# Kernel optimization log

Measured on AMD Instinct MI355X. Metric: run time of the kernel, lower is better.

## Reference

```python
import jax, jax.numpy as jnp
import numpy as np

N = 8192
D = 512


def setup_inputs() -> dict:
    key = jax.random.key(0)
    ks = jax.random.split(key, 7)
    X = jax.random.normal(ks[0], (N, D), dtype=jnp.float32)
    adj = jax.random.randint(ks[1], (N, N), 0, 2, dtype=jnp.int32)
    # guarantee at least one neighbor per row (self-loop) so softmax is defined
    adj = adj.at[jnp.arange(N), jnp.arange(N)].set(1)
    s = 1.0 / np.sqrt(D)
    Wq = jax.random.normal(ks[2], (D, D), dtype=jnp.float32) * s
    Wk = jax.random.normal(ks[3], (D, D), dtype=jnp.float32) * s
    Wv = jax.random.normal(ks[4], (D, D), dtype=jnp.float32) * s
    Wo = jax.random.normal(ks[5], (D, D), dtype=jnp.float32) * s
    bo = jnp.zeros((D,), dtype=jnp.float32)
    return {"X": X, "adj": adj, "Wq": Wq, "Wk": Wk, "Wv": Wv, "Wo": Wo, "bo": bo}


def reference(X, adj, Wq, Wk, Wv, Wo, bo):
    # torch Linear(no bias): y = x @ W.T
    Q = X @ Wq.T                                  # [N, D]
    K = X @ Wk.T                                  # [N, D]
    V = X @ Wv.T                                  # [N, D]
    scale = 1.0 / jnp.sqrt(jnp.asarray(D, X.dtype))
    scores = jnp.einsum('nd,md->nm', Q, K) * scale  # [N, N]
    scores = jnp.where(adj == 0, -jnp.inf, scores)
    attn = jax.nn.softmax(scores, axis=-1)          # [N, N]
    out = attn @ V                                  # [N, D]
    out = out @ Wo.T + bo                           # [N, D]
    return out
```

## Files before the change

### kernel.cpp

```cpp
#include <hip/hip_runtime.h>

namespace {

constexpr int NR = 8192;
constexpr int DD = 512;
constexpr int NSPLIT = 4;
constexpr int KVLEN = NR / NSPLIT;
constexpr int KT = 32;
constexpr int NT = KVLEN / KT;
constexpr int QB = 64;
constexpr float SCALE = 0.04419417382415922f;
constexpr float THR = 5.0f;

typedef __bf16 bf16x8 __attribute__((ext_vector_type(8)));
typedef __bf16 bf16x4 __attribute__((ext_vector_type(4)));
typedef float  f32x16 __attribute__((ext_vector_type(16)));

__device__ __forceinline__ f32x16 mfma(bf16x8 a, bf16x8 b, f32x16 c) {
    return __builtin_amdgcn_mfma_f32_32x32x16_bf16(a, b, c, 0, 0, 0);
}

__global__ void __launch_bounds__(256)
cast_kernel(const float* __restrict__ in, __bf16* __restrict__ out, int n8) {
    int i = blockIdx.x * 256 + threadIdx.x;
    if (i >= n8) return;
    const float4* p = (const float4*)(in + (size_t)i * 8);
    float4 v0 = p[0], v1 = p[1];
    bf16x8 o;
    o[0] = (__bf16)v0.x; o[1] = (__bf16)v0.y; o[2] = (__bf16)v0.z; o[3] = (__bf16)v0.w;
    o[4] = (__bf16)v1.x; o[5] = (__bf16)v1.y; o[6] = (__bf16)v1.z; o[7] = (__bf16)v1.w;
    *(bf16x8*)(out + (size_t)i * 8) = o;
}

template<bool FINAL>
__global__ void __launch_bounds__(256, 2)
gemm_kernel(const __bf16* __restrict__ A, const __bf16* __restrict__ B0,
            const __bf16* __restrict__ B1, const __bf16* __restrict__ B2,
            __bf16* __restrict__ C0, __bf16* __restrict__ C1, __bf16* __restrict__ C2,
            const float* __restrict__ bias, float* __restrict__ Cf)
{
    const __bf16* B = B0;
    __bf16* Cb = C0;
    if (!FINAL) {
        if (blockIdx.y == 1)      { B = B1; Cb = C1; }
        else if (blockIdx.y == 2) { B = B2; Cb = C2; }
    }
    __shared__ __bf16 As[128][72];
    __shared__ __bf16 Bs[128][72];
    const int t = threadIdx.x;
    const int w = t >> 6, lane = t & 63, lo = lane & 31, hi = lane >> 5;
    const int wm = w >> 1, wn = w & 1;
    const int bm = (blockIdx.x >> 2) * 128;
    const int bn = (blockIdx.x & 3) * 128;

    f32x16 acc[2][2];
    #pragma unroll
    for (int a = 0; a < 2; ++a)
        #pragma unroll
        for (int b = 0; b < 2; ++b)
            #pragma unroll
            for (int r = 0; r < 16; ++r) acc[a][b][r] = 0.f;

    for (int k0 = 0; k0 < DD; k0 += 64) {
        __syncthreads();
        #pragma unroll
        for (int pp = 0; pp < 2; ++pp) {
            int r = pp * 64 + (t >> 2), c = (t & 3) * 16;
            *(bf16x8*)&As[r][c]     = *(const bf16x8*)(A + (size_t)(bm + r) * DD + k0 + c);
            *(bf16x8*)&As[r][c + 8] = *(const bf16x8*)(A + (size_t)(bm + r) * DD + k0 + c + 8);
            *(bf16x8*)&Bs[r][c]     = *(const bf16x8*)(B + (size_t)(bn + r) * DD + k0 + c);
            *(bf16x8*)&Bs[r][c + 8] = *(const bf16x8*)(B + (size_t)(bn + r) * DD + k0 + c + 8);
        }
        __syncthreads();
        #pragma unroll
        for (int ks = 0; ks < 4; ++ks) {
            bf16x8 a0 = *(const bf16x8*)&As[wm * 64 + lo][ks * 16 + hi * 8];
            bf16x8 a1 = *(const bf16x8*)&As[wm * 64 + 32 + lo][ks * 16 + hi * 8];
            bf16x8 b0 = *(const bf16x8*)&Bs[wn * 64 + lo][ks * 16 + hi * 8];
            bf16x8 b1 = *(const bf16x8*)&Bs[wn * 64 + 32 + lo][ks * 16 + hi * 8];
            acc[0][0] = mfma(a0, b0, acc[0][0]);
            acc[0][1] = mfma(a0, b1, acc[0][1]);
            acc[1][0] = mfma(a1, b0, acc[1][0]);
            acc[1][1] = mfma(a1, b1, acc[1][1]);
        }
    }
    #pragma unroll
    for (int mi = 0; mi < 2; ++mi)
        #pragma unroll
        for (int ni = 0; ni < 2; ++ni) {
            int col = bn + wn * 64 + ni * 32 + lo;
            float bv = 0.f;
            if (FINAL) bv = bias[col];
            #pragma unroll
            for (int r = 0; r < 16; ++r) {
                int row = bm + wm * 64 + mi * 32 + (r & 3) + 8 * (r >> 2) + 4 * hi;
                if (FINAL) Cf[(size_t)row * DD + col] = acc[mi][ni][r] + bv;
                else       Cb[(size_t)row * DD + col] = (__bf16)acc[mi][ni][r];
            }
        }
}

__global__ void __launch_bounds__(256)
transpose_kernel(const __bf16* __restrict__ V, __bf16* __restrict__ Vt) {
    __shared__ __bf16 tile[64][72];
    const int t = threadIdx.x;
    const int rb = blockIdx.x * 64;
    const int cb = blockIdx.y * 64;
    #pragma unroll
    for (int pp = 0; pp < 2; ++pp) {
        int r = pp * 32 + (t >> 3), c = (t & 7) * 8;
        *(bf16x8*)&tile[r][c] = *(const bf16x8*)(V + (size_t)(rb + r) * DD + cb + c);
    }
    __syncthreads();
    #pragma unroll
    for (int pp = 0; pp < 2; ++pp) {
        int dd = pp * 32 + (t >> 3), co = (t & 7) * 8;
        bf16x8 o;
        #pragma unroll
        for (int j = 0; j < 8; ++j) o[j] = tile[co + j][dd];
        *(bf16x8*)(Vt + (size_t)(cb + dd) * NR + rb + co) = o;
    }
}

__global__ void __launch_bounds__(256, 2)
flash_kernel(const __bf16* __restrict__ Qg, const __bf16* __restrict__ Kg,
             const __bf16* __restrict__ Vt, const int* __restrict__ adj,
             __bf16* __restrict__ Opart, float* __restrict__ lse)
{
    __shared__ __bf16 Sp[4][QB][40];
    __shared__ __bf16 Pl[QB][40];
    __shared__ float  fl[QB];
    __shared__ float  ll[QB];
    __shared__ int    flg[4];

    const int t = threadIdx.x;
    const int w = t >> 6, lane = t & 63, lo = lane & 31, hi = lane >> 5;
    const int qblk = blockIdx.x * QB;
    const int split = blockIdx.y;
    const int kv0 = split * KVLEN;

    bf16x8 qa[2][8];
    #pragma unroll
    for (int mi = 0; mi < 2; ++mi)
        #pragma unroll
        for (int ks = 0; ks < 8; ++ks)
            qa[mi][ks] = *(const bf16x8*)(Qg + (size_t)(qblk + mi * 32 + lo) * DD + w * 128 + ks * 16 + hi * 8);

    f32x16 O[2][2][2];
    #pragma unroll
    for (int h = 0; h < 2; ++h)
        #pragma unroll
        for (int a = 0; a < 2; ++a)
            #pragma unroll
            for (int b = 0; b < 2; ++b)
                #pragma unroll
                for (int r = 0; r < 16; ++r) O[h][a][b][r] = 0.f;

    const __bf16* Kl = Kg + (size_t)(kv0 + lo) * DD + w * 128 + hi * 8;
    const __bf16* Vbase = Vt + (size_t)(w * 128 + lo) * NR + kv0 + hi * 8;

    const int qo = w * 16 + (lane >> 2);
    const int c8 = (lane & 3) * 8;
    const int* adjp = adj + (size_t)(qblk + qo) * NR + kv0 + c8;
    int4 aA = *(const int4*)adjp;
    int4 aB = *(const int4*)(adjp + 4);

    float m_run = -1e30f, l_run = 0.f;

    for (int tl = 0; tl < NT; ++tl) {
        f32x16 St0, St1;
        #pragma unroll
        for (int r = 0; r < 16; ++r) { St0[r] = 0.f; St1[r] = 0.f; }
        #pragma unroll
        for (int ks = 0; ks < 8; ++ks) {
            bf16x8 kb = *(const bf16x8*)(Kl + ks * 16);
            St0 = mfma(kb, qa[0][ks], St0);
            St1 = mfma(kb, qa[1][ks], St1);
        }
        Kl += KT * DD;
        #pragma unroll
        for (int g = 0; g < 4; ++g) {
            bf16x4 v0, v1;
            #pragma unroll
            for (int j = 0; j < 4; ++j) { v0[j] = (__bf16)St0[4 * g + j]; v1[j] = (__bf16)St1[4 * g + j]; }
            *(bf16x4*)&Sp[w][lo][8 * g + 4 * hi]      = v0;
            *(bf16x4*)&Sp[w][32 + lo][8 * g + 4 * hi] = v1;
        }
        __syncthreads();
        {
            bf16x8 p0 = *(const bf16x8*)&Sp[0][qo][c8];
            bf16x8 p1 = *(const bf16x8*)&Sp[1][qo][c8];
            bf16x8 p2 = *(const bf16x8*)&Sp[2][qo][c8];
            bf16x8 p3 = *(const bf16x8*)&Sp[3][qo][c8];
            int am[8] = {aA.x, aA.y, aA.z, aA.w, aB.x, aB.y, aB.z, aB.w};
            float s[8];
            #pragma unroll
            for (int i = 0; i < 8; ++i) {
                float v = ((float)p0[i] + (float)p1[i] + (float)p2[i] + (float)p3[i]) * SCALE;
                s[i] = (am[i] != 0) ? v : -1e30f;
            }
            float mx = s[0];
            #pragma unroll
            for (int i = 1; i < 8; ++i) mx = fmaxf(mx, s[i]);
            mx = fmaxf(mx, __shfl_xor(mx, 1));
            mx = fmaxf(mx, __shfl_xor(mx, 2));
            bool need = mx > m_run + THR;
            float m_new = need ? mx : m_run;
            float f = need ? __expf(m_run - m_new) : 1.f;
            float lsum = 0.f;
            bf16x8 pb;
            #pragma unroll
            for (int i = 0; i < 8; ++i) {
                float pv = __expf(s[i] - m_new);
                lsum += pv;
                pb[i] = (__bf16)pv;
            }
            lsum += __shfl_xor(lsum, 1);
            lsum += __shfl_xor(lsum, 2);
            l_run = l_run * f + lsum;
            m_run = m_new;
            *(bf16x8*)&Pl[qo][c8] = pb;
            if ((lane & 3) == 0) fl[qo] = f;
            unsigned long long bal = __ballot(need);
            if (lane == 0) flg[w] = (bal != 0ull) ? 1 : 0;
            int nxt = (tl + 1 < NT) ? (tl + 1) * KT : 0;
            aA = *(const int4*)(adjp + nxt);
            aB = *(const int4*)(adjp + nxt + 4);
        }
        __syncthreads();
        if (flg[0] | flg[1] | flg[2] | flg[3]) {
            #pragma unroll
            for (int mi = 0; mi < 2; ++mi)
                #pragma unroll
                for (int g = 0; g < 4; ++g) {
                    float4 fv = *(const float4*)&fl[mi * 32 + 8 * g + 4 * hi];
                    #pragma unroll
                    for (int j = 0; j < 4; ++j) {
                        float fac = (&fv.x)[j];
                        #pragma unroll
                        for (int h = 0; h < 2; ++h)
                            #pragma unroll
                            for (int ni = 0; ni < 2; ++ni)
                                O[h][mi][ni][g * 4 + j] *= fac;
                    }
                }
        }
        bf16x8 pa[2][2];
        #pragma unroll
        for (int mi = 0; mi < 2; ++mi)
            #pragma unroll
            for (int ks = 0; ks < 2; ++ks)
                pa[mi][ks] = *(const bf16x8*)&Pl[mi * 32 + lo][ks * 16 + hi * 8];
        const int vofs = tl * KT;
        #pragma unroll
        for (int h = 0; h < 2; ++h)
            #pragma unroll
            for (int ni = 0; ni < 2; ++ni) {
                const __bf16* vp = Vbase + (size_t)(h * 64 + ni * 32) * NR + vofs;
                bf16x8 vb0 = *(const bf16x8*)(vp);
                bf16x8 vb1 = *(const bf16x8*)(vp + 16);
                O[h][0][ni] = mfma(pa[0][0], vb0, O[h][0][ni]);
                O[h][1][ni] = mfma(pa[1][0], vb0, O[h][1][ni]);
                O[h][0][ni] = mfma(pa[0][1], vb1, O[h][0][ni]);
                O[h][1][ni] = mfma(pa[1][1], vb1, O[h][1][ni]);
            }
    }
    if ((lane & 3) == 0) {
        ll[qo] = l_run;
        lse[(size_t)split * NR + qblk + qo] = m_run + __logf(l_run);
    }
    __syncthreads();
    #pragma unroll
    for (int mi = 0; mi < 2; ++mi)
        #pragma unroll
        for (int g = 0; g < 4; ++g) {
            float4 lv = *(const float4*)&ll[mi * 32 + 8 * g + 4 * hi];
            #pragma unroll
            for (int j = 0; j < 4; ++j) {
                float inv = 1.f / (&lv.x)[j];
                int row = qblk + mi * 32 + 8 * g + 4 * hi + j;
                #pragma unroll
                for (int h = 0; h < 2; ++h)
                    #pragma unroll
                    for (int ni = 0; ni < 2; ++ni) {
                        int col = w * 128 + h * 64 + ni * 32 + lo;
                        Opart[(size_t)split * NR * DD + (size_t)row * DD + col] =
                            (__bf16)(O[h][mi][ni][g * 4 + j] * inv);
                    }
            }
        }
}

__global__ void __launch_bounds__(256)
merge_kernel(const __bf16* __restrict__ Opart, const float* __restrict__ lse,
             __bf16* __restrict__ attn)
{
    int idx = blockIdx.x * 256 + threadIdx.x;
    int q = idx >> 6;
    int c = (idx & 63) * 8;
    float l0 = lse[q], l1 = lse[NR + q], l2 = lse[2 * NR + q], l3 = lse[3 * NR + q];
    float M = fmaxf(fmaxf(l0, l1), fmaxf(l2, l3));
    float w0 = __expf(l0 - M), w1 = __expf(l1 - M), w2 = __expf(l2 - M), w3 = __expf(l3 - M);
    float Winv = 1.f / (w0 + w1 + w2 + w3);
    const size_t base = (size_t)q * DD + c;
    const size_t stride = (size_t)NR * DD;
    bf16x8 o0 = *(const bf16x8*)(Opart + base);
    bf16x8 o1 = *(const bf16x8*)(Opart + stride + base);
    bf16x8 o2 = *(const bf16x8*)(Opart + 2 * stride + base);
    bf16x8 o3 = *(const bf16x8*)(Opart + 3 * stride + base);
    bf16x8 o;
    #pragma unroll
    for (int i = 0; i < 8; ++i)
        o[i] = (__bf16)((w0 * (float)o0[i] + w1 * (float)o1[i] +
                         w2 * (float)o2[i] + w3 * (float)o3[i]) * Winv);
    *(bf16x8*)(attn + base) = o;
}

}

extern "C" void kernel_launch(void* const* d_in, const int* in_sizes, int n_in,
                              void* d_out, int out_size, void* d_ws, size_t ws_size,
                              hipStream_t stream)
{
    (void)in_sizes; (void)n_in; (void)out_size; (void)ws_size;
    const float* X  = (const float*)d_in[0];
    const int*   adj = (const int*)d_in[1];
    const float* Wq = (const float*)d_in[2];
    const float* Wk = (const float*)d_in[3];
    const float* Wv = (const float*)d_in[4];
    const float* Wo = (const float*)d_in[5];
    const float* bo = (const float*)d_in[6];
    float* out = (float*)d_out;

    char* ws = (char*)d_ws;
    __bf16* Xb   = (__bf16*)(ws + 0);
    __bf16* Att  = (__bf16*)(ws + 0);
    __bf16* Wqb  = (__bf16*)(ws + 8388608);
    __bf16* Wkb  = (__bf16*)(ws + 8912896);
    __bf16* Wvb  = (__bf16*)(ws + 9437184);
    __bf16* Wob  = (__bf16*)(ws + 9961472);
    __bf16* Qb   = (__bf16*)(ws + 10485760);
    __bf16* Kb   = (__bf16*)(ws + 18874368);
    __bf16* Vb   = (__bf16*)(ws + 27262976);
    __bf16* Vtb  = (__bf16*)(ws + 35651584);
    __bf16* Op   = (__bf16*)(ws + 44040192);
    float*  lseb = (float*)(ws + 77594624);

    cast_kernel<<<2048, 256, 0, stream>>>(X,  Xb,  NR * DD / 8);
    cast_kernel<<<128,  256, 0, stream>>>(Wq, Wqb, DD * DD / 8);
    cast_kernel<<<128,  256, 0, stream>>>(Wk, Wkb, DD * DD / 8);
    cast_kernel<<<128,  256, 0, stream>>>(Wv, Wvb, DD * DD / 8);
    cast_kernel<<<128,  256, 0, stream>>>(Wo, Wob, DD * DD / 8);

    gemm_kernel<false><<<dim3(256, 3), 256, 0, stream>>>(Xb, Wqb, Wkb, Wvb,
                                                         Qb, Kb, Vb, nullptr, nullptr);
    transpose_kernel<<<dim3(128, 8), 256, 0, stream>>>(Vb, Vtb);
    flash_kernel<<<dim3(128, NSPLIT), 256, 0, stream>>>(Qb, Kb, Vtb, adj, Op, lseb);
    merge_kernel<<<2048, 256, 0, stream>>>(Op, lseb, Att);
    gemm_kernel<true><<<dim3(256, 1), 256, 0, stream>>>(Att, Wob, nullptr, nullptr,
                                                        nullptr, nullptr, nullptr, bo, out);
}
```

Before: 472.5 us.

## Stage K and V tiles through swizzled LDS via async global_load_lds double buffering

The flash kernel now loads K tiles (double-buffered, prefetching the next tile) and V tiles into XOR-swizzled shared memory using global_load_lds DMA, with explicit vmcnt waits and raw barriers in place of __syncthreads. This is meant to hide global memory latency on the K and V fetches and overlap them with the MFMA work. The adjacency prefetch is also moved earlier in the loop. The extra LDS use forces occupancy down to one block per CU via launch bounds. The hand-counted vmcnt values are fragile and must match the exact number of outstanding loads.

After: 527.0 us. 11.5% more time.

```diff
diff --git a/kernel.cpp b/kernel.cpp
--- a/kernel.cpp
+++ b/kernel.cpp
@@ -18,6 +18,12 @@
 
 __device__ __forceinline__ f32x16 mfma(bf16x8 a, bf16x8 b, f32x16 c) {
     return __builtin_amdgcn_mfma_f32_32x32x16_bf16(a, b, c, 0, 0, 0);
+}
+
+typedef const __attribute__((address_space(1))) void g_void;
+typedef __attribute__((address_space(3))) void l_void;
+__device__ __forceinline__ void lds_dma16(const void* g, void* l) {
+    __builtin_amdgcn_global_load_lds((g_void*)g, (l_void*)l, 16, 0, 0);
 }
 
 __global__ void __launch_bounds__(256)
@@ -122,11 +128,13 @@
     }
 }
 
-__global__ void __launch_bounds__(256, 2)
+__global__ void __launch_bounds__(256, 1)
 flash_kernel(const __bf16* __restrict__ Qg, const __bf16* __restrict__ Kg,
              const __bf16* __restrict__ Vt, const int* __restrict__ adj,
              __bf16* __restrict__ Opart, float* __restrict__ lse)
 {
+    __shared__ __bf16 Ksw[2][4][KT][128];
+    __shared__ __bf16 Vsw[4][128][KT];
     __shared__ __bf16 Sp[4][QB][40];
     __shared__ __bf16 Pl[QB][40];
     __shared__ float  fl[QB];
@@ -156,28 +164,57 @@
                 #pragma unroll
                 for (int r = 0; r < 16; ++r) O[h][a][b][r] = 0.f;
 
-    const __bf16* Kl = Kg + (size_t)(kv0 + lo) * DD + w * 128 + hi * 8;
-    const __bf16* Vbase = Vt + (size_t)(w * 128 + lo) * NR + kv0 + hi * 8;
-
     const int qo = w * 16 + (lane >> 2);
     const int c8 = (lane & 3) * 8;
     const int* adjp = adj + (size_t)(qblk + qo) * NR + kv0 + c8;
+
+    const int l16 = lane & 15, lr4 = lane >> 4;
+    const int l4  = lane & 3,  lr2 = lane >> 2;
+
+    #pragma unroll
+    for (int i = 0; i < 8; ++i) {
+        int r = i * 4 + lr4;
+        int g = l16 ^ (r & 7);
+        lds_dma16(Kg + (size_t)(kv0 + r) * DD + w * 128 + g * 8, &Ksw[0][w][i * 4][0]);
+    }
     int4 aA = *(const int4*)adjp;
     int4 aB = *(const int4*)(adjp + 4);
 
     float m_run = -1e30f, l_run = 0.f;
 
     for (int tl = 0; tl < NT; ++tl) {
+        const int cb = tl & 1, nb = cb ^ 1;
+        const int kvb = kv0 + tl * KT;
+        const int tn = (tl + 1 == NT) ? 0 : tl + 1;
+        const int kvn = kv0 + tn * KT;
+
+        #pragma unroll
+        for (int i = 0; i < 8; ++i) {
+            int r = i * 16 + lr2;
+            int g = l4 ^ ((r >> 1) & 3);
+            lds_dma16(Vt + (size_t)(w * 128 + r) * NR + kvb + g * 8, &Vsw[w][i * 16][0]);
+        }
+        #pragma unroll
+        for (int i = 0; i < 8; ++i) {
+            int r = i * 4 + lr4;
+            int g = l16 ^ (r & 7);
+            lds_dma16(Kg + (size_t)(kvn + r) * DD + w * 128 + g * 8, &Ksw[nb][w][i * 4][0]);
+        }
+        int4 naA = *(const int4*)(adjp + tn * KT);
+        int4 naB = *(const int4*)(adjp + tn * KT + 4);
+
+        asm volatile("s_waitcnt vmcnt(18)" ::: "memory");
+
         f32x16 St0, St1;
         #pragma unroll
         for (int r = 0; r < 16; ++r) { St0[r] = 0.f; St1[r] = 0.f; }
         #pragma unroll
         for (int ks = 0; ks < 8; ++ks) {
-            bf16x8 kb = *(const bf16x8*)(Kl + ks * 16);
+            int cK = ((2 * ks + hi) ^ (lo & 7)) * 8;
+            bf16x8 kb = *(const bf16x8*)&Ksw[cb][w][lo][cK];
             St0 = mfma(kb, qa[0][ks], St0);
             St1 = mfma(kb, qa[1][ks], St1);
         }
-        Kl += KT * DD;
         #pragma unroll
         for (int g = 0; g < 4; ++g) {
             bf16x4 v0, v1;
@@ -186,7 +223,8 @@
             *(bf16x4*)&Sp[w][lo][8 * g + 4 * hi]      = v0;
             *(bf16x4*)&Sp[w][32 + lo][8 * g + 4 * hi] = v1;
         }
-        __syncthreads();
+        asm volatile("s_waitcnt lgkmcnt(0)\n\ts_barrier" ::: "memory");
+
         {
             bf16x8 p0 = *(const bf16x8*)&Sp[0][qo][c8];
             bf16x8 p1 = *(const bf16x8*)&Sp[1][qo][c8];
@@ -223,11 +261,10 @@
             if ((lane & 3) == 0) fl[qo] = f;
             unsigned long long bal = __ballot(need);
             if (lane == 0) flg[w] = (bal != 0ull) ? 1 : 0;
-            int nxt = (tl + 1 < NT) ? (tl + 1) * KT : 0;
-            aA = *(const int4*)(adjp + nxt);
-            aB = *(const int4*)(adjp + nxt + 4);
-        }
-        __syncthreads();
+            aA = naA; aB = naB;
+        }
+        asm volatile("s_waitcnt lgkmcnt(0)\n\ts_barrier" ::: "memory");
+
         if (flg[0] | flg[1] | flg[2] | flg[3]) {
             #pragma unroll
             for (int mi = 0; mi < 2; ++mi)
@@ -251,18 +288,22 @@
             #pragma unroll
             for (int ks = 0; ks < 2; ++ks)
                 pa[mi][ks] = *(const bf16x8*)&Pl[mi * 32 + lo][ks * 16 + hi * 8];
-        const int vofs = tl * KT;
+
+        asm volatile("s_waitcnt vmcnt(8)" ::: "memory");
+
         #pragma unroll
         for (int h = 0; h < 2; ++h)
             #pragma unroll
             for (int ni = 0; ni < 2; ++ni) {
-                const __bf16* vp = Vbase + (size_t)(h * 64 + ni * 32) * NR + vofs;
-                bf16x8 vb0 = *(const bf16x8*)(vp);
-                bf16x8 vb1 = *(const bf16x8*)(vp + 16);
-                O[h][0][ni] = mfma(pa[0][0], vb0, O[h][0][ni]);
-                O[h][1][ni] = mfma(pa[1][0], vb0, O[h][1][ni]);
-                O[h][0][ni] = mfma(pa[0][1], vb1, O[h][0][ni]);
-                O[h][1][ni] = mfma(pa[1][1], vb1, O[h][1][ni]);
+                const int dr = h * 64 + ni * 32 + lo;
+                const int sw = (dr >> 1) & 3;
+                #pragma unroll
+                for (int ks = 0; ks < 2; ++ks) {
+                    int cV = ((2 * ks + hi) ^ sw) * 8;
+                    bf16x8 vb = *(const bf16x8*)&Vsw[w][dr][cV];
+                    O[h][0][ni] = mfma(pa[0][ks], vb, O[h][0][ni]);
+                    O[h][1][ni] = mfma(pa[1][ks], vb, O[h][1][ni]);
+                }
             }
     }
     if ((lane & 3) == 0) {
```

## Pad K and V^T strides, remap flash blocks by XCD, prefetch adjacency two tiles ahead

Applied to the files above, without the earlier changes.

K is stored with a padded row stride of 528 and V^T with 8208, so the strided per-lane loads in the flash kernel stop hitting the same cache channels and banks. The flash grid becomes 1-D, with block IDs remapped so each pair of XCDs handles one KV split, keeping that split's K/V slice in one L2. The adjacency mask loads are double-buffered two tiles ahead to hide global latency. The workspace layout is rearranged: V shares space with Opart, which is safe only because V is consumed by the transpose before the flash kernel writes Opart.

Measured after the change: 421.7 us. -10.7%, faster.

```diff
diff --git a/kernel.cpp b/kernel.cpp
--- a/kernel.cpp
+++ b/kernel.cpp
@@ -4,6 +4,8 @@
 
 constexpr int NR = 8192;
 constexpr int DD = 512;
+constexpr int LDK = 528;
+constexpr int LDV = 8208;
 constexpr int NSPLIT = 4;
 constexpr int KVLEN = NR / NSPLIT;
 constexpr int KT = 32;
@@ -41,8 +43,9 @@
 {
     const __bf16* B = B0;
     __bf16* Cb = C0;
+    int ldc = DD;
     if (!FINAL) {
-        if (blockIdx.y == 1)      { B = B1; Cb = C1; }
+        if (blockIdx.y == 1)      { B = B1; Cb = C1; ldc = LDK; }
         else if (blockIdx.y == 2) { B = B2; Cb = C2; }
     }
     __shared__ __bf16 As[128][72];
@@ -95,7 +98,7 @@
             for (int r = 0; r < 16; ++r) {
                 int row = bm + wm * 64 + mi * 32 + (r & 3) + 8 * (r >> 2) + 4 * hi;
                 if (FINAL) Cf[(size_t)row * DD + col] = acc[mi][ni][r] + bv;
-                else       Cb[(size_t)row * DD + col] = (__bf16)acc[mi][ni][r];
+                else       Cb[(size_t)row * ldc + col] = (__bf16)acc[mi][ni][r];
             }
         }
 }
@@ -118,7 +121,7 @@
         bf16x8 o;
         #pragma unroll
         for (int j = 0; j < 8; ++j) o[j] = tile[co + j][dd];
-        *(bf16x8*)(Vt + (size_t)(cb + dd) * NR + rb + co) = o;
+        *(bf16x8*)(Vt + (size_t)(cb + dd) * LDV + rb + co) = o;
     }
 }
 
@@ -135,8 +138,11 @@
 
     const int t = threadIdx.x;
     const int w = t >> 6, lane = t & 63, lo = lane & 31, hi = lane >> 5;
-    const int qblk = blockIdx.x * QB;
-    const int split = blockIdx.y;
+    const int bid = blockIdx.x;
+    const int xcd = bid & 7;
+    const int j8 = bid >> 3;
+    const int split = xcd >> 1;
+    const int qblk = (((xcd & 1) << 6) | j8) * QB;
     const int kv0 = split * KVLEN;
 
     bf16x8 qa[2][8];
@@ -156,14 +162,16 @@
                 #pragma unroll
                 for (int r = 0; r < 16; ++r) O[h][a][b][r] = 0.f;
 
-    const __bf16* Kl = Kg + (size_t)(kv0 + lo) * DD + w * 128 + hi * 8;
-    const __bf16* Vbase = Vt + (size_t)(w * 128 + lo) * NR + kv0 + hi * 8;
+    const __bf16* Kl = Kg + (size_t)(kv0 + lo) * LDK + w * 128 + hi * 8;
+    const __bf16* Vbase = Vt + (size_t)(w * 128 + lo) * LDV + kv0 + hi * 8;
 
     const int qo = w * 16 + (lane >> 2);
     const int c8 = (lane & 3) * 8;
     const int* adjp = adj + (size_t)(qblk + qo) * NR + kv0 + c8;
     int4 aA = *(const int4*)adjp;
     int4 aB = *(const int4*)(adjp + 4);
+    int4 bA = *(const int4*)(adjp + KT);
+    int4 bB = *(const int4*)(adjp + KT + 4);
 
     float m_run = -1e30f, l_run = 0.f;
 
@@ -177,12 +185,12 @@
             St0 = mfma(kb, qa[0][ks], St0);
             St1 = mfma(kb, qa[1][ks], St1);
         }
-        Kl += KT * DD;
+        Kl += (size_t)KT * LDK;
         #pragma unroll
         for (int g = 0; g < 4; ++g) {
             bf16x4 v0, v1;
             #pragma unroll
-            for (int j = 0; j < 4; ++j) { v0[j] = (__bf16)St0[4 * g + j]; v1[j] = (__bf16)St1[4 * g + j]; }
+            for (int jj = 0; jj < 4; ++jj) { v0[jj] = (__bf16)St0[4 * g + jj]; v1[jj] = (__bf16)St1[4 * g + jj]; }
             *(bf16x4*)&Sp[w][lo][8 * g + 4 * hi]      = v0;
             *(bf16x4*)&Sp[w][32 + lo][8 * g + 4 * hi] = v1;
         }
@@ -223,9 +231,10 @@
             if ((lane & 3) == 0) fl[qo] = f;
             unsigned long long bal = __ballot(need);
             if (lane == 0) flg[w] = (bal != 0ull) ? 1 : 0;
-            int nxt = (tl + 1 < NT) ? (tl + 1) * KT : 0;
-            aA = *(const int4*)(adjp + nxt);
-            aB = *(const int4*)(adjp + nxt + 4);
+            aA = bA; aB = bB;
+            int nxt = (tl + 2 < NT) ? (tl + 2) * KT : 0;
+            bA = *(const int4*)(adjp + nxt);
+            bB = *(const int4*)(adjp + nxt + 4);
         }
         __syncthreads();
         if (flg[0] | flg[1] | flg[2] | flg[3]) {
@@ -235,13 +244,13 @@
                 for (int g = 0; g < 4; ++g) {
                     float4 fv = *(const float4*)&fl[mi * 32 + 8 * g + 4 * hi];
                     #pragma unroll
-                    for (int j = 0; j < 4; ++j) {
-                        float fac = (&fv.x)[j];
+                    for (int jj = 0; jj < 4; ++jj) {
+                        float fac = (&fv.x)[jj];
                         #pragma unroll
                         for (int h = 0; h < 2; ++h)
                             #pragma unroll
                             for (int ni = 0; ni < 2; ++ni)
-                                O[h][mi][ni][g * 4 + j] *= fac;
+                                O[h][mi][ni][g * 4 + jj] *= fac;
                     }
                 }
         }
@@ -256,7 +265,7 @@
         for (int h = 0; h < 2; ++h)
             #pragma unroll
             for (int ni = 0; ni < 2; ++ni) {
-                const __bf16* vp = Vbase + (size_t)(h * 64 + ni * 32) * NR + vofs;
+                const __bf16* vp = Vbase + (size_t)(h * 64 + ni * 32) * LDV + vofs;
                 bf16x8 vb0 = *(const bf16x8*)(vp);
                 bf16x8 vb1 = *(const bf16x8*)(vp + 16);
                 O[h][0][ni] = mfma(pa[0][0], vb0, O[h][0][ni]);
@@ -276,16 +285,16 @@
         for (int g = 0; g < 4; ++g) {
             float4 lv = *(const float4*)&ll[mi * 32 + 8 * g + 4 * hi];
             #pragma unroll
-            for (int j = 0; j < 4; ++j) {
-                float inv = 1.f / (&lv.x)[j];
-                int row = qblk + mi * 32 + 8 * g + 4 * hi + j;
+            for (int jj = 0; jj < 4; ++jj) {
+                float inv = 1.f / (&lv.x)[jj];
+                int row = qblk + mi * 32 + 8 * g + 4 * hi + jj;
                 #pragma unroll
                 for (int h = 0; h < 2; ++h)
                     #pragma unroll
                     for (int ni = 0; ni < 2; ++ni) {
                         int col = w * 128 + h * 64 + ni * 32 + lo;
                         Opart[(size_t)split * NR * DD + (size_t)row * DD + col] =
-                            (__bf16)(O[h][mi][ni][g * 4 + j] * inv);
+                            (__bf16)(O[h][mi][ni][g * 4 + jj] * inv);
                     }
             }
         }
@@ -340,11 +349,11 @@
     __bf16* Wvb  = (__bf16*)(ws + 9437184);
     __bf16* Wob  = (__bf16*)(ws + 9961472);
     __bf16* Qb   = (__bf16*)(ws + 10485760);
-    __bf16* Kb   = (__bf16*)(ws + 18874368);
-    __bf16* Vb   = (__bf16*)(ws + 27262976);
-    __bf16* Vtb  = (__bf16*)(ws + 35651584);
-    __bf16* Op   = (__bf16*)(ws + 44040192);
-    float*  lseb = (float*)(ws + 77594624);
+    __bf16* Kp   = (__bf16*)(ws + 18874368);
+    __bf16* Vtb  = (__bf16*)(ws + 27525120);
+    __bf16* Vb   = (__bf16*)(ws + 35930112);
+    __bf16* Op   = (__bf16*)(ws + 35930112);
+    float*  lseb = (float*)(ws + 69484544);
 
     cast_kernel<<<2048, 256, 0, stream>>>(X,  Xb,  NR * DD / 8);
     cast_kernel<<<128,  256, 0, stream>>>(Wq, Wqb, DD * DD / 8);
@@ -353,9 +362,9 @@
     cast_kernel<<<128,  256, 0, stream>>>(Wo, Wob, DD * DD / 8);
 
     gemm_kernel<false><<<dim3(256, 3), 256, 0, stream>>>(Xb, Wqb, Wkb, Wvb,
-                                                         Qb, Kb, Vb, nullptr, nullptr);
+                                                         Qb, Kp, Vb, nullptr, nullptr);
     transpose_kernel<<<dim3(128, 8), 256, 0, stream>>>(Vb, Vtb);
-    flash_kernel<<<dim3(128, NSPLIT), 256, 0, stream>>>(Qb, Kb, Vtb, adj, Op, lseb);
+    flash_kernel<<<512, 256, 0, stream>>>(Qb, Kp, Vtb, adj, Op, lseb);
     merge_kernel<<<2048, 256, 0, stream>>>(Op, lseb, Att);
     gemm_kernel<true><<<dim3(256, 1), 256, 0, stream>>>(Att, Wob, nullptr, nullptr,
                                                         nullptr, nullptr, nullptr, bo, out);
```
